# Kernel optimization log

Hardware: AMD Instinct MI355X
Metric: run time of the kernel (lower is better)

## Reference

```python
import jax, jax.numpy as jnp
import numpy as np

N_STEPS = 2   # n_steps; n_head = 1 (module is only consistent for a single head)
NEG_SLOPE = 0.2


def setup_inputs() -> dict:
    key = jax.random.key(0)
    ks = jax.random.split(key, 6)
    B, C, N = 8, 2048, 2048  # N must equal input_dim (coefs*out broadcast requirement)
    s = 1.0 / np.sqrt(C).astype(np.float32)
    x = jax.random.normal(ks[0], (B, C, N), jnp.float32)
    Wa = jax.random.normal(ks[1], (C, C), jnp.float32) * s   # conv1x1, no bias
    Wb = jax.random.normal(ks[2], (C,), jnp.float32) * s     # conv1x1 -> 1 channel
    bb = jnp.zeros((1,), jnp.float32)
    Wc = jax.random.normal(ks[3], (C,), jnp.float32) * s
    bc = jnp.zeros((1,), jnp.float32)
    bias = jnp.zeros((C,), jnp.float32)                      # self.bias (zeros)
    return dict(x=x, Wa=Wa, Wb=Wb, bb=bb, Wc=Wc, bc=bc, bias=bias)


def _head_attention(out, Wa, Wb, bb, Wc, bc, bias):
    # dropout p=0.0 -> identity
    h = jnp.einsum('oc,bcn->bon', Wa, out)            # [B,C,N] conv1x1 projection
    t1 = jnp.einsum('c,bcn->bn', Wb, h) + bb          # [B,N]
    t2 = jnp.einsum('c,bcn->bn', Wc, h) + bc          # [B,N]
    z = t1[:, None, :] + t2[:, :, None]               # [B,N,N] additive outer-sum
    z = jnp.where(z >= 0, z, NEG_SLOPE * z)           # leaky_relu(0.2)
    # torch F.softmax with no dim on a 3D tensor uses legacy dim=0 (batch dim)
    coefs = jax.nn.softmax(z, axis=0)
    re = coefs * h + bias                             # bias broadcasts over last axis
    return re                                         # [B,N,N] (== [B,C,N] since N==C)


def reference(x, Wa, Wb, bb, Wc, bc, bias):
    out = x
    for _ in range(N_STEPS):
        # n_head == 1: stack of one head then mean is the head itself
        out = _head_attention(out, Wa, Wb, bb, Wc, bc, bias)
    return out
```

## Files before the change

kernel.cpp:

```cpp
#include <hip/hip_runtime.h>
#include <hip/hip_bf16.h>

typedef unsigned short ushort_t;
typedef __attribute__((ext_vector_type(8))) short bf16x8;
typedef __attribute__((ext_vector_type(4))) float f32x4;
typedef __attribute__((ext_vector_type(8))) unsigned short u16x8;
typedef __attribute__((ext_vector_type(4))) unsigned short u16x4;

#define NDIM 2048
#define BDIM 8

__device__ __forceinline__ float bf2f(unsigned short u) {
  union { unsigned int i; float f; } v; v.i = ((unsigned int)u) << 16; return v.f;
}
__device__ __forceinline__ unsigned short f2bf(float f) {
  union { float f; unsigned int i; } v; v.f = f;
  unsigned int x = v.i;
  x += 0x7fffu + ((x >> 16) & 1u);
  return (unsigned short)(x >> 16);
}

__device__ __forceinline__ void gload16(const void* g, void* l) {
  __builtin_amdgcn_global_load_lds(
      (const __attribute__((address_space(1))) void*)g,
      (__attribute__((address_space(3))) void*)l,
      16, 0, 0);
}

__global__ __launch_bounds__(256) void convert_bf16(const float* __restrict__ src,
                                                    unsigned short* __restrict__ dst, int n) {
  int i = (blockIdx.x * 256 + threadIdx.x) * 4;
  if (i < n) {
    f32x4 v = *(const f32x4*)&src[i];
    u16x4 w;
    #pragma unroll
    for (int k = 0; k < 4; ++k) w[k] = f2bf(v[k]);
    *(u16x4*)&dst[i] = w;
  }
}

__global__ __launch_bounds__(256) void transpose_convert(const float* __restrict__ x,
                                                         unsigned short* __restrict__ dst) {
  __shared__ float tile[64][65];
  const int b  = blockIdx.z;
  const int n0 = blockIdx.x * 64;
  const int c0 = blockIdx.y * 64;
  const int tr = threadIdx.x >> 4;
  const int tc = threadIdx.x & 15;
  const float* src = x + ((size_t)b * NDIM + c0) * NDIM + n0;
  #pragma unroll
  for (int p = 0; p < 4; ++p) {
    int r = p * 16 + tr;
    f32x4 v = *(const f32x4*)&src[(size_t)r * NDIM + tc * 4];
    #pragma unroll
    for (int k = 0; k < 4; ++k) tile[r][tc * 4 + k] = v[k];
  }
  __syncthreads();
  unsigned short* d = dst + ((size_t)b * NDIM + n0) * NDIM + c0;
  #pragma unroll
  for (int p = 0; p < 4; ++p) {
    int r = p * 16 + tr;
    u16x4 w;
    #pragma unroll
    for (int k = 0; k < 4; ++k) w[k] = f2bf(tile[tc * 4 + k][r]);
    *(u16x4*)&d[(size_t)r * NDIM + tc * 4] = w;
  }
}

__global__ __launch_bounds__(256) void weff1(const float* __restrict__ Wa,
                                             const float* __restrict__ Wb,
                                             const float* __restrict__ Wc,
                                             float* __restrict__ part) {
  int c  = blockIdx.x * 256 + threadIdx.x;
  int o0 = blockIdx.y * 128;
  float ab = 0.f, ac = 0.f;
  for (int o = o0; o < o0 + 128; ++o) {
    float w = Wa[(size_t)o * NDIM + c];
    ab = fmaf(Wb[o], w, ab);
    ac = fmaf(Wc[o], w, ac);
  }
  part[(size_t)(blockIdx.y * 2 + 0) * NDIM + c] = ab;
  part[(size_t)(blockIdx.y * 2 + 1) * NDIM + c] = ac;
}
__global__ __launch_bounds__(256) void weff2(const float* __restrict__ part,
                                             float* __restrict__ wbe, float* __restrict__ wce) {
  int c = blockIdx.x * 256 + threadIdx.x;
  float ab = 0.f, ac = 0.f;
  #pragma unroll
  for (int i = 0; i < 16; ++i) {
    ab += part[(size_t)(i * 2 + 0) * NDIM + c];
    ac += part[(size_t)(i * 2 + 1) * NDIM + c];
  }
  wbe[c] = ab; wce[c] = ac;
}

__global__ __launch_bounds__(256) void t_kernel(const unsigned short* __restrict__ curT,
                                                const float* __restrict__ wbe,
                                                const float* __restrict__ wce,
                                                const float* __restrict__ bb,
                                                const float* __restrict__ bc,
                                                float* __restrict__ t1, float* __restrict__ t2) {
  int row  = blockIdx.x * 4 + (threadIdx.x >> 6);
  int lane = threadIdx.x & 63;
  const unsigned short* r = curT + (size_t)row * NDIM;
  float a1 = 0.f, a2 = 0.f;
  #pragma unroll
  for (int p = 0; p < 4; ++p) {
    int c0 = p * 512 + lane * 8;
    u16x8 v = *(const u16x8*)&r[c0];
    f32x4 w1a = *(const f32x4*)&wbe[c0];
    f32x4 w1b = *(const f32x4*)&wbe[c0 + 4];
    f32x4 w2a = *(const f32x4*)&wce[c0];
    f32x4 w2b = *(const f32x4*)&wce[c0 + 4];
    #pragma unroll
    for (int j = 0; j < 4; ++j) {
      float xv = bf2f(v[j]);
      a1 = fmaf(w1a[j], xv, a1);
      a2 = fmaf(w2a[j], xv, a2);
    }
    #pragma unroll
    for (int j = 0; j < 4; ++j) {
      float xv = bf2f(v[4 + j]);
      a1 = fmaf(w1b[j], xv, a1);
      a2 = fmaf(w2b[j], xv, a2);
    }
  }
  #pragma unroll
  for (int off = 32; off > 0; off >>= 1) {
    a1 += __shfl_xor(a1, off);
    a2 += __shfl_xor(a2, off);
  }
  if (lane == 0) { t1[row] = a1 + bb[0]; t2[row] = a2 + bc[0]; }
}

__global__ __launch_bounds__(256) void s_kernel(const float* __restrict__ t1,
                                                const float* __restrict__ t2,
                                                float* __restrict__ S) {
  int n = blockIdx.x * 256 + threadIdx.x;
  int o = blockIdx.y;
  float acc = 0.f;
  #pragma unroll
  for (int b = 0; b < BDIM; ++b) {
    float z = t1[b * NDIM + n] + t2[b * NDIM + o];
    z = z >= 0.f ? z : 0.2f * z;
    acc += __expf(z);
  }
  S[(size_t)o * NDIM + n] = __logf(acc);
}

__global__ __launch_bounds__(512, 2) void gemm_fused(
    const unsigned short* __restrict__ A,
    const unsigned short* __restrict__ Bt,
    const float* __restrict__ t1, const float* __restrict__ t2,
    const float* __restrict__ S,  const float* __restrict__ bias,
    unsigned short* __restrict__ outT,
    float* __restrict__ outF,
    int write_f32) {
  __shared__ __align__(16) unsigned short sbuf[4 * 16384];

  const int tid  = threadIdx.x;
  const int lane = tid & 63;
  const int w    = tid >> 6;
  const int wr   = w >> 2;
  const int wc   = w & 3;
  const int bn0  = blockIdx.x * 256;
  const int bm0  = blockIdx.y * 256;
  const int bz   = blockIdx.z;
  const unsigned short* Bb = Bt + (size_t)bz * NDIM * NDIM;

  f32x4 acc[8][4];
  #pragma unroll
  for (int m = 0; m < 8; ++m)
    #pragma unroll
    for (int n = 0; n < 4; ++n) acc[m][n] = (f32x4){0.f, 0.f, 0.f, 0.f};

  const int sr = lane >> 2;
  const int sc = lane & 3;
  const int r0 = (w * 2 + 0) * 16 + sr;
  const int r1 = (w * 2 + 1) * 16 + sr;
  const int sg = sc ^ ((r0 >> 1) & 3);
  const unsigned short* a0 = A  + (size_t)(bm0 + r0) * NDIM + sg * 8;
  const unsigned short* a1 = A  + (size_t)(bm0 + r1) * NDIM + sg * 8;
  const unsigned short* b0 = Bb + (size_t)(bn0 + r0) * NDIM + sg * 8;
  const unsigned short* b1 = Bb + (size_t)(bn0 + r1) * NDIM + sg * 8;

  auto stageA = [&](int kt, int buf) {
    gload16(a0 + kt, &sbuf[buf * 16384 + (w * 2 + 0) * 512]);
    gload16(a1 + kt, &sbuf[buf * 16384 + (w * 2 + 1) * 512]);
  };
  auto stageB = [&](int kt, int buf) {
    gload16(b0 + kt, &sbuf[buf * 16384 + 8192 + (w * 2 + 0) * 512]);
    gload16(b1 + kt, &sbuf[buf * 16384 + 8192 + (w * 2 + 1) * 512]);
  };

  const int fr = lane & 15;
  const int fs = lane >> 4;
  const int sp = (fs ^ ((fr >> 1) & 3)) * 8;

  stageA(0, 0);  stageB(0, 0);
  stageA(32, 1); stageB(32, 1);
  stageA(64, 2); stageB(64, 2);
  asm volatile("s_waitcnt vmcnt(8)" ::: "memory");
  __builtin_amdgcn_s_barrier();

  for (int t4 = 0; t4 < 64; t4 += 4) {
    #pragma unroll
    for (int u = 0; u < 4; ++u) {
      const int t  = t4 + u;
      const int cb = u;
      const int nb = (u + 3) & 3;
      const int tc = (t + 3 > 63) ? 63 : (t + 3);
      const int ktn = tc * 32;
      const unsigned short* Ab = &sbuf[cb * 16384];
      const unsigned short* Bl = &sbuf[cb * 16384 + 8192];

      bf16x8 av[4], bv[4];
      #pragma unroll
      for (int m = 0; m < 4; ++m)
        av[m] = *(const bf16x8*)&Ab[(wr * 128 + m * 16 + fr) * 32 + sp];
      #pragma unroll
      for (int n = 0; n < 4; ++n)
        bv[n] = *(const bf16x8*)&Bl[(wc * 64 + n * 16 + fr) * 32 + sp];
      stageA(ktn, nb);
      __builtin_amdgcn_sched_barrier(0);
      __builtin_amdgcn_s_barrier();
      asm volatile("s_waitcnt lgkmcnt(0)" ::: "memory");
      __builtin_amdgcn_sched_barrier(0);
      __builtin_amdgcn_s_setprio(1);
      #pragma unroll
      for (int m = 0; m < 4; ++m)
        #pragma unroll
        for (int n = 0; n < 4; ++n)
          acc[m][n] = __builtin_amdgcn_mfma_f32_16x16x32_bf16(av[m], bv[n], acc[m][n], 0, 0, 0);
      __builtin_amdgcn_s_setprio(0);
      __builtin_amdgcn_sched_barrier(0);
      __builtin_amdgcn_s_barrier();

      #pragma unroll
      for (int m = 0; m < 4; ++m)
        av[m] = *(const bf16x8*)&Ab[(wr * 128 + (m + 4) * 16 + fr) * 32 + sp];
      stageB(ktn, nb);
      __builtin_amdgcn_sched_barrier(0);
      __builtin_amdgcn_s_barrier();
      asm volatile("s_waitcnt lgkmcnt(0)" ::: "memory");
      __builtin_amdgcn_sched_barrier(0);
      __builtin_amdgcn_s_setprio(1);
      #pragma unroll
      for (int m = 0; m < 4; ++m)
        #pragma unroll
        for (int n = 0; n < 4; ++n)
          acc[m + 4][n] = __builtin_amdgcn_mfma_f32_16x16x32_bf16(av[m], bv[n], acc[m + 4][n], 0, 0, 0);
      __builtin_amdgcn_s_setprio(0);
      __builtin_amdgcn_sched_barrier(0);
      asm volatile("s_waitcnt vmcnt(8)" ::: "memory");
      __builtin_amdgcn_s_barrier();
    }
  }

  float* sT1f = (float*)&sbuf[0];
  float* sT2f = sT1f + 256;
  if (tid < 256) sT1f[tid] = t1[bz * NDIM + bn0 + tid];
  else           sT2f[tid - 256] = t2[bz * NDIM + bm0 + (tid - 256)];
  __syncthreads();

  const int lr4 = fs * 4;
  #pragma unroll
  for (int m = 0; m < 8; ++m) {
    #pragma unroll
    for (int n = 0; n < 4; ++n) {
      const int oo = wr * 128 + m * 16 + lr4;
      const int nn = wc * 64 + n * 16 + fr;
      const int o  = bm0 + oo;
      const int ng = bn0 + nn;
      const float tz1  = sT1f[nn];
      const float bval = bias[ng];
      if (write_f32) {
        #pragma unroll
        for (int r = 0; r < 4; ++r) {
          float z = tz1 + sT2f[oo + r];
          z = z >= 0.f ? z : 0.2f * z;
          float coef = __expf(z - S[(size_t)(o + r) * NDIM + ng]);
          outF[(size_t)bz * NDIM * NDIM + (size_t)(o + r) * NDIM + ng] =
              fmaf(coef, acc[m][n][r], bval);
        }
      } else {
        u16x4 wv;
        #pragma unroll
        for (int r = 0; r < 4; ++r) {
          float z = tz1 + sT2f[oo + r];
          z = z >= 0.f ? z : 0.2f * z;
          float coef = __expf(z - S[(size_t)(o + r) * NDIM + ng]);
          wv[r] = f2bf(fmaf(coef, acc[m][n][r], bval));
        }
        *(u16x4*)&outT[(size_t)bz * NDIM * NDIM + (size_t)ng * NDIM + o] = wv;
      }
    }
  }
}

extern "C" void kernel_launch(void* const* d_in, const int* in_sizes, int n_in,
                              void* d_out, int out_size, void* d_ws, size_t ws_size,
                              hipStream_t stream) {
  const float* x    = (const float*)d_in[0];
  const float* Wa   = (const float*)d_in[1];
  const float* Wb   = (const float*)d_in[2];
  const float* bb   = (const float*)d_in[3];
  const float* Wc   = (const float*)d_in[4];
  const float* bc   = (const float*)d_in[5];
  const float* bias = (const float*)d_in[6];
  float* out = (float*)d_out;

  char* ws = (char*)d_ws;
  unsigned short* curA = (unsigned short*)ws; ws += (size_t)BDIM * NDIM * NDIM * 2;
  unsigned short* curB = (unsigned short*)ws; ws += (size_t)BDIM * NDIM * NDIM * 2;
  unsigned short* WaB  = (unsigned short*)ws; ws += (size_t)NDIM * NDIM * 2;
  float* t1   = (float*)ws; ws += (size_t)BDIM * NDIM * 4;
  float* t2   = (float*)ws; ws += (size_t)BDIM * NDIM * 4;
  float* wbe  = (float*)ws; ws += NDIM * 4;
  float* wce  = (float*)ws; ws += NDIM * 4;
  float* part = (float*)ws; ws += (size_t)32 * NDIM * 4;
  float* S    = (float*)ws; ws += (size_t)NDIM * NDIM * 4;

  convert_bf16<<<4096, 256, 0, stream>>>(Wa, WaB, NDIM * NDIM);
  transpose_convert<<<dim3(32, 32, BDIM), 256, 0, stream>>>(x, curA);
  weff1<<<dim3(8, 16), 256, 0, stream>>>(Wa, Wb, Wc, part);
  weff2<<<8, 256, 0, stream>>>(part, wbe, wce);

  for (int step = 0; step < 2; ++step) {
    const unsigned short* cur = step ? curB : curA;
    t_kernel<<<(BDIM * NDIM) / 4, 256, 0, stream>>>(cur, wbe, wce, bb, bc, t1, t2);
    s_kernel<<<dim3(NDIM / 256, NDIM), 256, 0, stream>>>(t1, t2, S);
    gemm_fused<<<dim3(8, 8, BDIM), 512, 0, stream>>>(
        WaB, cur, t1, t2, S, bias, curB, out, step);
  }
}
```

Before: 388.8 us.

## Shrink GEMM tile to 256x128 with triple-buffered LDS and higher occupancy

The fused GEMM tile drops from 256x256 to 256x128, each wave now owns a 64x64 sub-tile, and the grid doubles along N. LDS staging goes from a 4-deep to a 3-deep ring of smaller buffers, with one barrier per k-step instead of two and a separate epilogue step for the last k-tile. Launch bounds now ask for 4 blocks per CU so more blocks can be resident to hide latency. In exchange, each block reuses less data per tile, so more operand traffic goes from global memory to LDS, and the shallower prefetch depth gives less time to hide load latency.

After: 419.5 us. 7.9% more time.

```diff
diff --git a/kernel.cpp b/kernel.cpp
--- a/kernel.cpp
+++ b/kernel.cpp
@@ -148,7 +148,7 @@
   S[(size_t)o * NDIM + n] = __logf(acc);
 }
 
-__global__ __launch_bounds__(512, 2) void gemm_fused(
+__global__ __launch_bounds__(512, 4) void gemm_fused(
     const unsigned short* __restrict__ A,
     const unsigned short* __restrict__ Bt,
     const float* __restrict__ t1, const float* __restrict__ t2,
@@ -156,74 +156,65 @@
     unsigned short* __restrict__ outT,
     float* __restrict__ outF,
     int write_f32) {
-  __shared__ __align__(16) unsigned short sbuf[4 * 16384];
+  __shared__ __align__(16) unsigned short sbuf[3 * 12288];
 
   const int tid  = threadIdx.x;
   const int lane = tid & 63;
   const int w    = tid >> 6;
-  const int wr   = w >> 2;
-  const int wc   = w & 3;
-  const int bn0  = blockIdx.x * 256;
+  const int wr   = w >> 1;
+  const int wc   = w & 1;
+  const int bn0  = blockIdx.x * 128;
   const int bm0  = blockIdx.y * 256;
   const int bz   = blockIdx.z;
   const unsigned short* Bb = Bt + (size_t)bz * NDIM * NDIM;
 
-  f32x4 acc[8][4];
-  #pragma unroll
-  for (int m = 0; m < 8; ++m)
+  f32x4 acc[4][4];
+  #pragma unroll
+  for (int m = 0; m < 4; ++m)
     #pragma unroll
     for (int n = 0; n < 4; ++n) acc[m][n] = (f32x4){0.f, 0.f, 0.f, 0.f};
 
   const int sr = lane >> 2;
   const int sc = lane & 3;
-  const int r0 = (w * 2 + 0) * 16 + sr;
-  const int r1 = (w * 2 + 1) * 16 + sr;
-  const int sg = sc ^ ((r0 >> 1) & 3);
-  const unsigned short* a0 = A  + (size_t)(bm0 + r0) * NDIM + sg * 8;
-  const unsigned short* a1 = A  + (size_t)(bm0 + r1) * NDIM + sg * 8;
-  const unsigned short* b0 = Bb + (size_t)(bn0 + r0) * NDIM + sg * 8;
-  const unsigned short* b1 = Bb + (size_t)(bn0 + r1) * NDIM + sg * 8;
-
-  auto stageA = [&](int kt, int buf) {
-    gload16(a0 + kt, &sbuf[buf * 16384 + (w * 2 + 0) * 512]);
-    gload16(a1 + kt, &sbuf[buf * 16384 + (w * 2 + 1) * 512]);
-  };
-  auto stageB = [&](int kt, int buf) {
-    gload16(b0 + kt, &sbuf[buf * 16384 + 8192 + (w * 2 + 0) * 512]);
-    gload16(b1 + kt, &sbuf[buf * 16384 + 8192 + (w * 2 + 1) * 512]);
+  const int sg = sc ^ ((sr >> 1) & 3);
+  const unsigned short* a0 = A  + (size_t)(bm0 + (w * 2 + 0) * 16 + sr) * NDIM + sg * 8;
+  const unsigned short* a1 = A  + (size_t)(bm0 + (w * 2 + 1) * 16 + sr) * NDIM + sg * 8;
+  const unsigned short* b0 = Bb + (size_t)(bn0 + w * 16 + sr) * NDIM + sg * 8;
+
+  auto stage = [&](int kt, int buf) {
+    gload16(a0 + kt, &sbuf[buf * 12288 + (w * 2 + 0) * 512]);
+    gload16(a1 + kt, &sbuf[buf * 12288 + (w * 2 + 1) * 512]);
+    gload16(b0 + kt, &sbuf[buf * 12288 + 8192 + w * 512]);
   };
 
   const int fr = lane & 15;
   const int fs = lane >> 4;
   const int sp = (fs ^ ((fr >> 1) & 3)) * 8;
 
-  stageA(0, 0);  stageB(0, 0);
-  stageA(32, 1); stageB(32, 1);
-  stageA(64, 2); stageB(64, 2);
-  asm volatile("s_waitcnt vmcnt(8)" ::: "memory");
+  stage(0, 0);
+  stage(32, 1);
+  asm volatile("s_waitcnt vmcnt(3)" ::: "memory");
   __builtin_amdgcn_s_barrier();
 
-  for (int t4 = 0; t4 < 64; t4 += 4) {
-    #pragma unroll
-    for (int u = 0; u < 4; ++u) {
-      const int t  = t4 + u;
+  for (int t3 = 0; t3 < 63; t3 += 3) {
+    #pragma unroll
+    for (int u = 0; u < 3; ++u) {
+      const int t  = t3 + u;
       const int cb = u;
-      const int nb = (u + 3) & 3;
-      const int tc = (t + 3 > 63) ? 63 : (t + 3);
-      const int ktn = tc * 32;
-      const unsigned short* Ab = &sbuf[cb * 16384];
-      const unsigned short* Bl = &sbuf[cb * 16384 + 8192];
+      const int nb = (u + 2) % 3;
+      const int tc = (t + 2 > 63) ? 63 : (t + 2);
+      const unsigned short* Ab = &sbuf[cb * 12288];
+      const unsigned short* Bl = &sbuf[cb * 12288 + 8192];
 
       bf16x8 av[4], bv[4];
       #pragma unroll
       for (int m = 0; m < 4; ++m)
-        av[m] = *(const bf16x8*)&Ab[(wr * 128 + m * 16 + fr) * 32 + sp];
+        av[m] = *(const bf16x8*)&Ab[(wr * 64 + m * 16 + fr) * 32 + sp];
       #pragma unroll
       for (int n = 0; n < 4; ++n)
         bv[n] = *(const bf16x8*)&Bl[(wc * 64 + n * 16 + fr) * 32 + sp];
-      stageA(ktn, nb);
+      stage(tc * 32, nb);
       __builtin_amdgcn_sched_barrier(0);
-      __builtin_amdgcn_s_barrier();
       asm volatile("s_waitcnt lgkmcnt(0)" ::: "memory");
       __builtin_amdgcn_sched_barrier(0);
       __builtin_amdgcn_s_setprio(1);
@@ -234,41 +225,42 @@
           acc[m][n] = __builtin_amdgcn_mfma_f32_16x16x32_bf16(av[m], bv[n], acc[m][n], 0, 0, 0);
       __builtin_amdgcn_s_setprio(0);
       __builtin_amdgcn_sched_barrier(0);
-      __builtin_amdgcn_s_barrier();
-
-      #pragma unroll
-      for (int m = 0; m < 4; ++m)
-        av[m] = *(const bf16x8*)&Ab[(wr * 128 + (m + 4) * 16 + fr) * 32 + sp];
-      stageB(ktn, nb);
-      __builtin_amdgcn_sched_barrier(0);
-      __builtin_amdgcn_s_barrier();
-      asm volatile("s_waitcnt lgkmcnt(0)" ::: "memory");
-      __builtin_amdgcn_sched_barrier(0);
-      __builtin_amdgcn_s_setprio(1);
-      #pragma unroll
-      for (int m = 0; m < 4; ++m)
-        #pragma unroll
-        for (int n = 0; n < 4; ++n)
-          acc[m + 4][n] = __builtin_amdgcn_mfma_f32_16x16x32_bf16(av[m], bv[n], acc[m + 4][n], 0, 0, 0);
-      __builtin_amdgcn_s_setprio(0);
-      __builtin_amdgcn_sched_barrier(0);
-      asm volatile("s_waitcnt vmcnt(8)" ::: "memory");
+      asm volatile("s_waitcnt vmcnt(3)" ::: "memory");
       __builtin_amdgcn_s_barrier();
     }
   }
-
+  {
+    const unsigned short* Ab = &sbuf[0];
+    const unsigned short* Bl = &sbuf[8192];
+    bf16x8 av[4], bv[4];
+    #pragma unroll
+    for (int m = 0; m < 4; ++m)
+      av[m] = *(const bf16x8*)&Ab[(wr * 64 + m * 16 + fr) * 32 + sp];
+    #pragma unroll
+    for (int n = 0; n < 4; ++n)
+      bv[n] = *(const bf16x8*)&Bl[(wc * 64 + n * 16 + fr) * 32 + sp];
+    asm volatile("s_waitcnt lgkmcnt(0)" ::: "memory");
+    __builtin_amdgcn_sched_barrier(0);
+    #pragma unroll
+    for (int m = 0; m < 4; ++m)
+      #pragma unroll
+      for (int n = 0; n < 4; ++n)
+        acc[m][n] = __builtin_amdgcn_mfma_f32_16x16x32_bf16(av[m], bv[n], acc[m][n], 0, 0, 0);
+  }
+
+  __syncthreads();
   float* sT1f = (float*)&sbuf[0];
-  float* sT2f = sT1f + 256;
-  if (tid < 256) sT1f[tid] = t1[bz * NDIM + bn0 + tid];
-  else           sT2f[tid - 256] = t2[bz * NDIM + bm0 + (tid - 256)];
+  float* sT2f = sT1f + 128;
+  if (tid < 128) sT1f[tid] = t1[bz * NDIM + bn0 + tid];
+  else if (tid < 384) sT2f[tid - 128] = t2[bz * NDIM + bm0 + (tid - 128)];
   __syncthreads();
 
   const int lr4 = fs * 4;
   #pragma unroll
-  for (int m = 0; m < 8; ++m) {
+  for (int m = 0; m < 4; ++m) {
     #pragma unroll
     for (int n = 0; n < 4; ++n) {
-      const int oo = wr * 128 + m * 16 + lr4;
+      const int oo = wr * 64 + m * 16 + lr4;
       const int nn = wc * 64 + n * 16 + fr;
       const int o  = bm0 + oo;
       const int ng = bn0 + nn;
@@ -330,7 +322,7 @@
     const unsigned short* cur = step ? curB : curA;
     t_kernel<<<(BDIM * NDIM) / 4, 256, 0, stream>>>(cur, wbe, wce, bb, bc, t1, t2);
     s_kernel<<<dim3(NDIM / 256, NDIM), 256, 0, stream>>>(t1, t2, S);
-    gemm_fused<<<dim3(8, 8, BDIM), 512, 0, stream>>>(
+    gemm_fused<<<dim3(16, 8, BDIM), 512, 0, stream>>>(
         WaB, cur, t1, t2, S, bias, curB, out, step);
   }
 }
```
